# Kernel optimization log

Hardware: AMD Instinct MI355X
Metric: run time of the kernel (lower is better)

The kernel has to match this reference:

```python
import jax, jax.numpy as jnp
import numpy as np

D = 768  # in_channels == out_channels (forced by residual + shared LayerNorm)
B, S = 8, 2048


def setup_inputs() -> dict:
    key = jax.random.key(0)
    ks = jax.random.split(key, 5)
    x = jax.random.normal(ks[0], (B, S, D), dtype=jnp.float32)
    # LayerNorm params
    ln_g = jnp.ones((D,), dtype=jnp.float32)
    ln_b = jnp.zeros((D,), dtype=jnp.float32)
    # Q/K linear params (torch Linear: y = x @ W.T + b)
    scale = 1.0 / np.sqrt(D)
    Wq = jax.random.uniform(ks[1], (D, D), jnp.float32, -scale, scale)
    bq = jax.random.uniform(ks[2], (D,), jnp.float32, -scale, scale)
    Wk = jax.random.uniform(ks[3], (D, D), jnp.float32, -scale, scale)
    bk = jax.random.uniform(ks[4], (D,), jnp.float32, -scale, scale)
    return {"x": x, "ln_g": ln_g, "ln_b": ln_b, "Wq": Wq, "bq": bq, "Wk": Wk, "bk": bk}


def _layernorm(x, g, b, eps=1e-5):
    mu = jnp.mean(x, axis=-1, keepdims=True)
    var = jnp.mean(jnp.square(x - mu), axis=-1, keepdims=True)
    return (x - mu) * jax.lax.rsqrt(var + eps) * g + b


def reference(x, ln_g, ln_b, Wq, bq, Wk, bk):
    origin = x
    xn = _layernorm(x, ln_g, ln_b)
    Q = xn @ Wq.T + bq  # [B,S,D]
    K = xn @ Wk.T + bk  # [B,S,D]
    scores = jnp.einsum('bsd,btd->bst', Q, K) / jnp.sqrt(jnp.asarray(D, x.dtype))
    attn = jax.nn.softmax(scores, axis=-1)  # [B,S,S]
    out = jnp.einsum('bst,btd->bsd', attn, origin) + origin
    # note: original then computes relu(layernorm(out)) but returns `out` (dead code)
    return out
```

## Files before the change

### kernel.cpp

```cpp
#include <hip/hip_runtime.h>

typedef __bf16 bf16;
typedef __bf16 v8bf __attribute__((ext_vector_type(8)));
typedef __bf16 v4bf __attribute__((ext_vector_type(4)));
typedef float  v4f  __attribute__((ext_vector_type(4)));

__device__ __forceinline__ void gload_lds16(const void* g, void* l) {
    __builtin_amdgcn_global_load_lds(
        (const __attribute__((address_space(1))) void*)g,
        (__attribute__((address_space(3))) void*)l, 16, 0, 0);
}

#define MFMA16(a, b, c) __builtin_amdgcn_mfma_f32_16x16x32_bf16((a), (b), (c), 0, 0, 0)

__global__ __launch_bounds__(256)
void ln_cast(const float* __restrict__ x, const float* __restrict__ g,
             const float* __restrict__ b, bf16* __restrict__ xn,
             bf16* __restrict__ xv, float* __restrict__ L)
{
    const long row = blockIdx.x;
    const float* xr = x + row * 768;
    const int tid = threadIdx.x;
    const int wave = tid >> 6, lane = tid & 63;

    if (row < 64) L[row * 256 + tid] = 0.0f;

    float a0 = xr[tid], a1 = xr[tid + 256], a2 = xr[tid + 512];
    float s = a0 + a1 + a2;
    #pragma unroll
    for (int off = 32; off; off >>= 1) s += __shfl_xor(s, off);
    __shared__ float sh[4], sh2[4];
    if (!lane) sh[wave] = s;
    __syncthreads();
    const float mu = (sh[0] + sh[1] + sh[2] + sh[3]) * (1.0f / 768.0f);

    float d0 = a0 - mu, d1 = a1 - mu, d2 = a2 - mu;
    float ss = d0 * d0 + d1 * d1 + d2 * d2;
    #pragma unroll
    for (int off = 32; off; off >>= 1) ss += __shfl_xor(ss, off);
    if (!lane) sh2[wave] = ss;
    __syncthreads();
    const float var = (sh2[0] + sh2[1] + sh2[2] + sh2[3]) * (1.0f / 768.0f);
    const float rstd = rsqrtf(var + 1e-5f);

    bf16* xnr = xn + row * 768;
    bf16* xvr = xv + row * 768;
    xnr[tid]       = (bf16)(d0 * rstd * g[tid]       + b[tid]);
    xnr[tid + 256] = (bf16)(d1 * rstd * g[tid + 256] + b[tid + 256]);
    xnr[tid + 512] = (bf16)(d2 * rstd * g[tid + 512] + b[tid + 512]);
    xvr[tid]       = (bf16)a0;
    xvr[tid + 256] = (bf16)a1;
    xvr[tid + 512] = (bf16)a2;
}

__global__ __launch_bounds__(256)
void cvt_w(const float* __restrict__ Wq, const float* __restrict__ Wk,
           bf16* __restrict__ Wcat)
{
    const int z = blockIdx.y;
    const float* src = z ? Wk : Wq;
    bf16* dst = Wcat + (long)z * 768 * 768;
    const int i = (blockIdx.x * 256 + threadIdx.x) * 4;
    const float4 v = *(const float4*)(src + i);
    v4bf o = {(bf16)v.x, (bf16)v.y, (bf16)v.z, (bf16)v.w};
    *(v4bf*)(dst + i) = o;
}

__global__ __launch_bounds__(256)
void transpose_bf(const bf16* __restrict__ in, bf16* __restrict__ outT)
{
    __shared__ __attribute__((aligned(16))) bf16 tile[64 * 64];
    const int t0 = blockIdx.x * 64, d0 = blockIdx.y * 64;
    in   += (long)blockIdx.z * 2048 * 768;
    outT += (long)blockIdx.z * 768 * 2048;
    const int tid = threadIdx.x;

    #pragma unroll
    for (int it = 0; it < 2; ++it) {
        const int lin = it * 256 + tid;
        const int r = lin >> 3;
        const int g = lin & 7;
        const int pg = g ^ (r & 7) ^ ((r >> 3) & 7);
        v8bf v = *(const v8bf*)(in + (long)(t0 + r) * 768 + d0 + g * 8);
        *(v8bf*)(tile + r * 64 + pg * 8) = v;
    }
    __syncthreads();
    #pragma unroll
    for (int it = 0; it < 2; ++it) {
        const int lin = it * 256 + tid;
        const int dd = lin >> 3;
        const int tb = lin & 7;
        v8bf o;
        #pragma unroll
        for (int j = 0; j < 8; ++j) {
            const int t = tb * 8 + j;
            const int pg = (dd >> 3) ^ (t & 7) ^ ((t >> 3) & 7);
            o[j] = tile[t * 64 + pg * 8 + (dd & 7)];
        }
        *(v8bf*)(outT + (long)(d0 + dd) * 2048 + t0 + tb * 8) = o;
    }
}

__global__ __launch_bounds__(256)
void gemm_qk(const bf16* __restrict__ A, const bf16* __restrict__ W,
             const float* __restrict__ bq, const float* __restrict__ bk,
             float qscale, bf16* __restrict__ Qb, bf16* __restrict__ Kb)
{
    __shared__ __attribute__((aligned(16))) bf16 As[2][128 * 32];
    __shared__ __attribute__((aligned(16))) bf16 Bs[2][128 * 32];

    const int bx = blockIdx.x;
    const int r = bx & 7, j = bx >> 3;
    const int m0 = (r * 16 + j / 12) * 128;
    const int n0 = (j % 12) * 128;

    const int tid = threadIdx.x, wave = tid >> 6, lane = tid & 63;
    const bf16* Ab = A + (long)m0 * 768;
    const bf16* Bb = W + (long)n0 * 768;

    const int lrow = lane >> 2;
    const int lk   = (lane & 3) * 8;
    const int wm = (wave >> 1) * 64, wn = (wave & 1) * 64;
    const int lr = lane & 15, lq = lane >> 4;

    v4f acc[4][4] = {};

    for (int kk = 0; kk < 768; kk += 64) {
        #pragma unroll
        for (int p = 0; p < 2; ++p)
            #pragma unroll
            for (int it = 0; it < 2; ++it) {
                const int c = it * 4 + wave;
                const int row = c * 16 + lrow;
                gload_lds16(Ab + (long)row * 768 + kk + p * 32 + lk,
                            (char*)As[p] + c * 1024);
                gload_lds16(Bb + (long)row * 768 + kk + p * 32 + lk,
                            (char*)Bs[p] + c * 1024);
            }
        __syncthreads();

        #pragma unroll
        for (int p = 0; p < 2; ++p) {
            v8bf af[4], bfr[4];
            #pragma unroll
            for (int i = 0; i < 4; ++i)
                af[i] = *(const v8bf*)(As[p] + (wm + i * 16 + lr) * 32 + lq * 8);
            #pragma unroll
            for (int jj = 0; jj < 4; ++jj)
                bfr[jj] = *(const v8bf*)(Bs[p] + (wn + jj * 16 + lr) * 32 + lq * 8);
            #pragma unroll
            for (int i = 0; i < 4; ++i)
                #pragma unroll
                for (int jj = 0; jj < 4; ++jj)
                    acc[i][jj] = MFMA16(af[i], bfr[jj], acc[i][jj]);
        }
        __syncthreads();
    }

    const bool isQ = (n0 < 768);
    const float* bias = isQ ? bq : bk;
    const float sc = isQ ? qscale : 1.0f;
    bf16* C = isQ ? Qb : Kb;
    const int c0 = isQ ? n0 : n0 - 768;

    #pragma unroll
    for (int i = 0; i < 4; ++i) {
        #pragma unroll
        for (int rr = 0; rr < 4; ++rr) {
            const int row = m0 + wm + i * 16 + lq * 4 + rr;
            #pragma unroll
            for (int jj = 0; jj < 4; ++jj) {
                const int col = c0 + wn + jj * 16 + lr;
                C[(long)row * 768 + col] = (bf16)((acc[i][jj][rr] + bias[col]) * sc);
            }
        }
    }
}

__global__ __launch_bounds__(512, 2)
void gemm_scores(const bf16* __restrict__ Q, const bf16* __restrict__ K,
                 bf16* __restrict__ E, float* __restrict__ L)
{
    __shared__ __attribute__((aligned(16))) bf16 lds[2][32768];

    const int bx = blockIdx.x;
    const int batch = bx & 7, j = bx >> 3;
    const int m0 = (j >> 3) * 256, n0 = (j & 7) * 256;

    const bf16* Ag = Q + (long)batch * 2048 * 768 + (long)m0 * 768;
    const bf16* Bg = K + (long)batch * 2048 * 768 + (long)n0 * 768;
    bf16* C = E + (long)batch * 2048 * 2048;
    float* Lb = L + (long)batch * 2048;

    const int tid = threadIdx.x, wv = tid >> 6, lane = tid & 63;
    const int wr = wv >> 2, wc = wv & 3;
    const int lr = lane & 15, lq = lane >> 4;

    auto stA = [&](int bi, int h, int p, int kk) {
        const int lin = (wv * 2 + p) * 64 + lane;
        const int r = lin >> 3, ck = (lin & 7) ^ (r & 7);
        gload_lds16(Ag + (long)(h * 128 + r) * 768 + kk + ck * 8,
                    (char*)lds + bi * 65536 + h * 16384 + lin * 16);
    };
    auto stB = [&](int bi, int h, int p, int kk) {
        const int lin = (wv * 2 + p) * 64 + lane;
        const int r = lin >> 3, ck = (lin & 7) ^ (r & 7);
        gload_lds16(Bg + (long)(h * 128 + r) * 768 + kk + ck * 8,
                    (char*)lds + bi * 65536 + 32768 + h * 16384 + lin * 16);
    };

    v8bf a[4][2], b[2][2];
    v4f acc[2][2][4][2] = {};

    auto rdA = [&](const bf16* Ls, int mh) {
        #pragma unroll
        for (int i = 0; i < 4; ++i) {
            const int r = mh * 128 + wr * 64 + i * 16 + lr;
            #pragma unroll
            for (int s = 0; s < 2; ++s)
                a[i][s] = *(const v8bf*)(Ls + r * 64 + (((s * 4 + lq) ^ (r & 7)) << 3));
        }
    };
    auto rdB = [&](const bf16* Ls, int nh) {
        #pragma unroll
        for (int n = 0; n < 2; ++n) {
            const int r = nh * 128 + wc * 32 + n * 16 + lr;
            #pragma unroll
            for (int s = 0; s < 2; ++s)
                b[n][s] = *(const v8bf*)(Ls + 16384 + r * 64 + (((s * 4 + lq) ^ (r & 7)) << 3));
        }
    };
    auto mm = [&](v4f (&ac)[4][2]) {
        __builtin_amdgcn_s_setprio(1);
        #pragma unroll
        for (int s = 0; s < 2; ++s)
            #pragma unroll
            for (int i = 0; i < 4; ++i)
                #pragma unroll
                for (int n = 0; n < 2; ++n)
                    ac[i][n] = MFMA16(a[i][s], b[n][s], ac[i][n]);
        __builtin_amdgcn_s_setprio(0);
    };

    const int NT = 12;
    stA(0, 0, 0, 0); stA(0, 0, 1, 0); stB(0, 0, 0, 0); stB(0, 0, 1, 0);
    stA(0, 1, 0, 0); stA(0, 1, 1, 0); stB(0, 1, 0, 0); stB(0, 1, 1, 0);
    asm volatile("s_waitcnt vmcnt(4)" ::: "memory");
    __builtin_amdgcn_s_barrier();

    for (int t = 0; t < NT; ++t) {
        const int cur = t & 1, nxt = cur ^ 1;
        const int kk2 = (t + 1 < NT ? t + 1 : NT - 1) * 64;
        const bf16* Ls = lds[cur];

        rdA(Ls, 0); rdB(Ls, 0);
        stA(nxt, 0, 0, kk2); stA(nxt, 0, 1, kk2);
        __builtin_amdgcn_s_barrier();
        mm(acc[0][0]);
        asm volatile("s_waitcnt vmcnt(4)" ::: "memory");
        __builtin_amdgcn_s_barrier();

        rdA(Ls, 1);
        stB(nxt, 0, 0, kk2); stB(nxt, 0, 1, kk2);
        __builtin_amdgcn_s_barrier();
        mm(acc[1][0]);
        asm volatile("s_waitcnt vmcnt(4)" ::: "memory");
        __builtin_amdgcn_s_barrier();

        rdB(Ls, 1);
        stA(nxt, 1, 0, kk2); stA(nxt, 1, 1, kk2);
        __builtin_amdgcn_s_barrier();
        mm(acc[1][1]);
        __builtin_amdgcn_s_barrier();

        rdA(Ls, 0);
        stB(nxt, 1, 0, kk2); stB(nxt, 1, 1, kk2);
        __builtin_amdgcn_s_barrier();
        mm(acc[0][1]);
        asm volatile("s_waitcnt vmcnt(4)" ::: "memory");
        __builtin_amdgcn_s_barrier();
    }
    asm volatile("s_waitcnt vmcnt(0)" ::: "memory");

    #pragma unroll
    for (int mh = 0; mh < 2; ++mh)
    #pragma unroll
    for (int i = 0; i < 4; ++i) {
        #pragma unroll
        for (int rr = 0; rr < 4; ++rr) {
            const int row = m0 + mh * 128 + wr * 64 + i * 16 + lq * 4 + rr;
            float e[4], rs = 0.f;
            #pragma unroll
            for (int nh = 0; nh < 2; ++nh)
                #pragma unroll
                for (int n = 0; n < 2; ++n) {
                    e[nh * 2 + n] = __expf(acc[mh][nh][i][n][rr]);
                    rs += e[nh * 2 + n];
                }
            #pragma unroll
            for (int off = 1; off < 16; off <<= 1) rs += __shfl_xor(rs, off);
            if (lr == 0) atomicAdd(&Lb[row], rs);
            #pragma unroll
            for (int nh = 0; nh < 2; ++nh)
                #pragma unroll
                for (int n = 0; n < 2; ++n) {
                    const int col = n0 + nh * 128 + wc * 32 + n * 16 + lr;
                    C[(long)row * 2048 + col] = (bf16)e[nh * 2 + n];
                }
        }
    }
}

__global__ __launch_bounds__(512, 2)
void gemm_pv(const bf16* __restrict__ P, const bf16* __restrict__ VT,
             const float* __restrict__ L, const float* __restrict__ Xres,
             float* __restrict__ Out)
{
    __shared__ __attribute__((aligned(16))) bf16 lds[2][32768];

    const int bx = blockIdx.x;
    const int batch = bx & 7, j = bx >> 3;
    const int m0 = (j >> 1) * 128;
    const int n0 = (j & 1) * 384;

    const bf16* Ag = P  + (long)batch * 2048 * 2048 + (long)m0 * 2048;
    const bf16* Bg = VT + (long)batch * 768 * 2048  + (long)n0 * 2048;
    const float* Lb = L + (long)batch * 2048;
    const float* Xr = Xres + (long)batch * 2048 * 768;
    float* O = Out + (long)batch * 2048 * 768;

    const int tid = threadIdx.x, wv = tid >> 6, lane = tid & 63;
    const int wr = wv >> 2, wc = wv & 3;
    const int lr = lane & 15, lq = lane >> 4;

    auto stA = [&](int bi, int h, int kk) {
        const int lin = wv * 64 + lane;
        const int r = lin >> 3, ck = (lin & 7) ^ (r & 7);
        gload_lds16(Ag + (long)(h * 64 + r) * 2048 + kk + ck * 8,
                    (char*)lds + bi * 65536 + h * 8192 + lin * 16);
    };
    auto stB = [&](int bi, int h, int p, int kk) {
        const int lin = (wv * 3 + p) * 64 + lane;
        const int r = lin >> 3, ck = (lin & 7) ^ (r & 7);
        gload_lds16(Bg + (long)(h * 192 + r) * 2048 + kk + ck * 8,
                    (char*)lds + bi * 65536 + 16384 + h * 24576 + lin * 16);
    };

    v8bf a[2][2], b[3][2];
    v4f acc[2][2][2][3] = {};

    auto rdA = [&](const bf16* Ls, int mh) {
        #pragma unroll
        for (int i = 0; i < 2; ++i) {
            const int r = mh * 64 + wr * 32 + i * 16 + lr;
            #pragma unroll
            for (int s = 0; s < 2; ++s)
                a[i][s] = *(const v8bf*)(Ls + r * 64 + (((s * 4 + lq) ^ (r & 7)) << 3));
        }
    };
    auto rdB = [&](const bf16* Ls, int nh) {
        #pragma unroll
        for (int n = 0; n < 3; ++n) {
            const int r = nh * 192 + wc * 48 + n * 16 + lr;
            #pragma unroll
            for (int s = 0; s < 2; ++s)
                b[n][s] = *(const v8bf*)(Ls + 8192 + r * 64 + (((s * 4 + lq) ^ (r & 7)) << 3));
        }
    };
    auto mm = [&](v4f (&ac)[2][3]) {
        __builtin_amdgcn_s_setprio(1);
        #pragma unroll
        for (int s = 0; s < 2; ++s)
            #pragma unroll
            for (int i = 0; i < 2; ++i)
                #pragma unroll
                for (int n = 0; n < 3; ++n)
                    ac[i][n] = MFMA16(a[i][s], b[n][s], ac[i][n]);
        __builtin_amdgcn_s_setprio(0);
    };

    const int NT = 32;
    stA(0, 0, 0); stB(0, 0, 0, 0); stB(0, 0, 1, 0); stB(0, 0, 2, 0);
    stA(0, 1, 0); stB(0, 1, 0, 0); stB(0, 1, 1, 0); stB(0, 1, 2, 0);
    asm volatile("s_waitcnt vmcnt(4)" ::: "memory");
    __builtin_amdgcn_s_barrier();

    for (int t = 0; t < NT; ++t) {
        const int cur = t & 1, nxt = cur ^ 1;
        const int kk2 = (t + 1 < NT ? t + 1 : NT - 1) * 64;
        const bf16* Ls = lds[cur];

        rdA(Ls, 0); rdB(Ls, 0);
        stA(nxt, 0, kk2); stB(nxt, 0, 0, kk2);
        __builtin_amdgcn_s_barrier();
        mm(acc[0][0]);
        asm volatile("s_waitcnt vmcnt(5)" ::: "memory");
        __builtin_amdgcn_s_barrier();

        rdA(Ls, 1);
        stB(nxt, 0, 1, kk2); stB(nxt, 0, 2, kk2);
        __builtin_amdgcn_s_barrier();
        mm(acc[1][0]);
        asm volatile("s_waitcnt vmcnt(4)" ::: "memory");
        __builtin_amdgcn_s_barrier();

        rdB(Ls, 1);
        stA(nxt, 1, kk2); stB(nxt, 1, 0, kk2);
        __builtin_amdgcn_s_barrier();
        mm(acc[1][1]);
        __builtin_amdgcn_s_barrier();

        rdA(Ls, 0);
        stB(nxt, 1, 1, kk2); stB(nxt, 1, 2, kk2);
        __builtin_amdgcn_s_barrier();
        mm(acc[0][1]);
        asm volatile("s_waitcnt vmcnt(4)" ::: "memory");
        __builtin_amdgcn_s_barrier();
    }
    asm volatile("s_waitcnt vmcnt(0)" ::: "memory");

    #pragma unroll
    for (int mh = 0; mh < 2; ++mh)
    #pragma unroll
    for (int i = 0; i < 2; ++i) {
        #pragma unroll
        for (int rr = 0; rr < 4; ++rr) {
            const int row = m0 + mh * 64 + wr * 32 + i * 16 + lq * 4 + rr;
            const float invL = 1.0f / Lb[row];
            #pragma unroll
            for (int nh = 0; nh < 2; ++nh)
                #pragma unroll
                for (int n = 0; n < 3; ++n) {
                    const int col = n0 + nh * 192 + wc * 48 + n * 16 + lr;
                    const long idx = (long)row * 768 + col;
                    O[idx] = acc[mh][nh][i][n][rr] * invL + Xr[idx];
                }
        }
    }
}

extern "C" void kernel_launch(void* const* d_in, const int* in_sizes, int n_in,
                              void* d_out, int out_size, void* d_ws, size_t ws_size,
                              hipStream_t stream)
{
    const float* x    = (const float*)d_in[0];
    const float* ln_g = (const float*)d_in[1];
    const float* ln_b = (const float*)d_in[2];
    const float* Wq   = (const float*)d_in[3];
    const float* bq   = (const float*)d_in[4];
    const float* Wk   = (const float*)d_in[5];
    const float* bk   = (const float*)d_in[6];
    float* out = (float*)d_out;

    const long R = 8L * 2048;
    char* ws = (char*)d_ws;
    size_t off = 0;
    auto take = [&](size_t bytes) -> char* {
        char* p = ws + off;
        off += (bytes + 255) & ~(size_t)255;
        return p;
    };
    bf16*  xn   = (bf16*)take(R * 768 * 2);
    bf16*  xv   = (bf16*)take(R * 768 * 2);
    bf16*  Qb   = (bf16*)take(R * 768 * 2);
    bf16*  Kb   = (bf16*)take(R * 768 * 2);
    bf16*  Wcat = (bf16*)take(1536L * 768 * 2);
    float* Lrow = (float*)take(R * 4);
    bf16*  Sc   = (bf16*)take(8L * 2048 * 2048 * 2);

    ln_cast<<<R, 256, 0, stream>>>(x, ln_g, ln_b, xn, xv, Lrow);
    cvt_w<<<dim3(576, 2), 256, 0, stream>>>(Wq, Wk, Wcat);

    const float qscale = 0.036084391824351615f;
    gemm_qk<<<1536, 256, 0, stream>>>(xn, Wcat, bq, bk, qscale, Qb, Kb);

    bf16* xvT = xn;
    transpose_bf<<<dim3(32, 12, 8), 256, 0, stream>>>(xv, xvT);

    gemm_scores<<<512, 512, 0, stream>>>(Qb, Kb, Sc, Lrow);
    gemm_pv<<<256, 512, 0, stream>>>(Sc, xvT, Lrow, x, out);
}
```

Baseline: 312.1 us.

## Retile QK projection GEMM and software-pipeline LDS fragment reads across all GEMMs

The Q/K projection GEMM moves from a simple 128x128 double-buffered loop to a 128x384 tile with 512 threads, reusing the same swizzled 4-phase pipeline as the PV GEMM. In all three GEMMs, LDS fragment reads for the next phase are issued before the current MFMA block, including prefetching the next k-tile's first fragments, and some barriers are removed. The goal is to hide LDS read latency behind MFMAs and cut barrier stalls. The cost is more registers from the extra fragment buffers, and the vmcnt/barrier ordering needs care to stay correct.

```diff
diff --git a/kernel.cpp b/kernel.cpp
--- a/kernel.cpp
+++ b/kernel.cpp
@@ -101,61 +101,108 @@
     }
 }
 
-__global__ __launch_bounds__(256)
+__global__ __launch_bounds__(512, 2)
 void gemm_qk(const bf16* __restrict__ A, const bf16* __restrict__ W,
              const float* __restrict__ bq, const float* __restrict__ bk,
              float qscale, bf16* __restrict__ Qb, bf16* __restrict__ Kb)
 {
-    __shared__ __attribute__((aligned(16))) bf16 As[2][128 * 32];
-    __shared__ __attribute__((aligned(16))) bf16 Bs[2][128 * 32];
+    __shared__ __attribute__((aligned(16))) bf16 lds[2][32768];
 
     const int bx = blockIdx.x;
-    const int r = bx & 7, j = bx >> 3;
-    const int m0 = (r * 16 + j / 12) * 128;
-    const int n0 = (j % 12) * 128;
-
-    const int tid = threadIdx.x, wave = tid >> 6, lane = tid & 63;
-    const bf16* Ab = A + (long)m0 * 768;
-    const bf16* Bb = W + (long)n0 * 768;
-
-    const int lrow = lane >> 2;
-    const int lk   = (lane & 3) * 8;
-    const int wm = (wave >> 1) * 64, wn = (wave & 1) * 64;
+    const int wg = (bx & 7) * 64 + (bx >> 3);
+    const int m0 = (wg >> 2) * 128;
+    const int n0 = (wg & 3) * 384;
+
+    const bf16* Ag = A + (long)m0 * 768;
+    const bf16* Bg = W + (long)n0 * 768;
+
+    const int tid = threadIdx.x, wv = tid >> 6, lane = tid & 63;
+    const int wr = wv >> 2, wc = wv & 3;
     const int lr = lane & 15, lq = lane >> 4;
 
-    v4f acc[4][4] = {};
-
-    for (int kk = 0; kk < 768; kk += 64) {
-        #pragma unroll
-        for (int p = 0; p < 2; ++p)
-            #pragma unroll
-            for (int it = 0; it < 2; ++it) {
-                const int c = it * 4 + wave;
-                const int row = c * 16 + lrow;
-                gload_lds16(Ab + (long)row * 768 + kk + p * 32 + lk,
-                            (char*)As[p] + c * 1024);
-                gload_lds16(Bb + (long)row * 768 + kk + p * 32 + lk,
-                            (char*)Bs[p] + c * 1024);
-            }
-        __syncthreads();
-
-        #pragma unroll
-        for (int p = 0; p < 2; ++p) {
-            v8bf af[4], bfr[4];
-            #pragma unroll
-            for (int i = 0; i < 4; ++i)
-                af[i] = *(const v8bf*)(As[p] + (wm + i * 16 + lr) * 32 + lq * 8);
-            #pragma unroll
-            for (int jj = 0; jj < 4; ++jj)
-                bfr[jj] = *(const v8bf*)(Bs[p] + (wn + jj * 16 + lr) * 32 + lq * 8);
-            #pragma unroll
-            for (int i = 0; i < 4; ++i)
-                #pragma unroll
-                for (int jj = 0; jj < 4; ++jj)
-                    acc[i][jj] = MFMA16(af[i], bfr[jj], acc[i][jj]);
-        }
-        __syncthreads();
-    }
+    auto stA = [&](int bi, int h, int kk) {
+        const int lin = wv * 64 + lane;
+        const int r = lin >> 3, ck = (lin & 7) ^ (r & 7);
+        gload_lds16(Ag + (long)(h * 64 + r) * 768 + kk + ck * 8,
+                    (char*)lds + bi * 65536 + h * 8192 + lin * 16);
+    };
+    auto stB = [&](int bi, int h, int p, int kk) {
+        const int lin = (wv * 3 + p) * 64 + lane;
+        const int r = lin >> 3, ck = (lin & 7) ^ (r & 7);
+        gload_lds16(Bg + (long)(h * 192 + r) * 768 + kk + ck * 8,
+                    (char*)lds + bi * 65536 + 16384 + h * 24576 + lin * 16);
+    };
+
+    v8bf aS1[2][2], aS2[2][2], aS3[2][2], bS4[3][2], bS5[3][2];
+    v4f acc[2][2][2][3] = {};
+
+    auto rdA = [&](v8bf (&d)[2][2], const bf16* Ls, int mh) {
+        #pragma unroll
+        for (int i = 0; i < 2; ++i) {
+            const int r = mh * 64 + wr * 32 + i * 16 + lr;
+            #pragma unroll
+            for (int s = 0; s < 2; ++s)
+                d[i][s] = *(const v8bf*)(Ls + r * 64 + (((s * 4 + lq) ^ (r & 7)) << 3));
+        }
+    };
+    auto rdB = [&](v8bf (&d)[3][2], const bf16* Ls, int nh) {
+        #pragma unroll
+        for (int n = 0; n < 3; ++n) {
+            const int r = nh * 192 + wc * 48 + n * 16 + lr;
+            #pragma unroll
+            for (int s = 0; s < 2; ++s)
+                d[n][s] = *(const v8bf*)(Ls + 8192 + r * 64 + (((s * 4 + lq) ^ (r & 7)) << 3));
+        }
+    };
+    auto mm = [&](v8bf (&a)[2][2], v8bf (&b)[3][2], v4f (&ac)[2][3]) {
+        __builtin_amdgcn_s_setprio(1);
+        #pragma unroll
+        for (int s = 0; s < 2; ++s)
+            #pragma unroll
+            for (int i = 0; i < 2; ++i)
+                #pragma unroll
+                for (int n = 0; n < 3; ++n)
+                    ac[i][n] = MFMA16(a[i][s], b[n][s], ac[i][n]);
+        __builtin_amdgcn_s_setprio(0);
+    };
+
+    const int NT = 12;
+    stA(0, 0, 0); stB(0, 0, 0, 0); stB(0, 0, 1, 0); stB(0, 0, 2, 0);
+    stA(0, 1, 0); stB(0, 1, 0, 0); stB(0, 1, 1, 0); stB(0, 1, 2, 0);
+    asm volatile("s_waitcnt vmcnt(3)" ::: "memory");
+    __builtin_amdgcn_s_barrier();
+    rdA(aS1, lds[0], 0); rdB(bS4, lds[0], 0);
+
+    for (int t = 0; t < NT; ++t) {
+        const int cur = t & 1, nxt = cur ^ 1;
+        const int kk2 = (t + 1 < NT ? t + 1 : t) * 64;
+        const bf16* Ls = lds[cur];
+        const bf16* Ln = lds[nxt];
+
+        rdA(aS2, Ls, 1);
+        stA(nxt, 0, kk2);
+        mm(aS1, bS4, acc[0][0]);
+        asm volatile("s_waitcnt vmcnt(1)" ::: "memory");
+        __builtin_amdgcn_s_barrier();
+
+        rdB(bS5, Ls, 1);
+        stB(nxt, 0, 0, kk2); stB(nxt, 0, 1, kk2); stB(nxt, 0, 2, kk2);
+        mm(aS2, bS4, acc[1][0]);
+        __builtin_amdgcn_s_barrier();
+
+        rdA(aS3, Ls, 0);
+        stA(nxt, 1, kk2);
+        mm(aS2, bS5, acc[1][1]);
+        asm volatile("s_waitcnt vmcnt(1)" ::: "memory");
+        __builtin_amdgcn_s_barrier();
+
+        rdA(aS1, Ln, 0); rdB(bS4, Ln, 0);
+        stB(nxt, 1, 0, kk2); stB(nxt, 1, 1, kk2); stB(nxt, 1, 2, kk2);
+        mm(aS3, bS5, acc[0][1]);
+        asm volatile("s_waitcnt vmcnt(3)" ::: "memory");
+        __builtin_amdgcn_s_barrier();
+    }
+    asm volatile("s_waitcnt vmcnt(0)" ::: "memory");
 
     const bool isQ = (n0 < 768);
     const float* bias = isQ ? bq : bk;
@@ -164,15 +211,19 @@
     const int c0 = isQ ? n0 : n0 - 768;
 
     #pragma unroll
-    for (int i = 0; i < 4; ++i) {
+    for (int mh = 0; mh < 2; ++mh)
+    #pragma unroll
+    for (int i = 0; i < 2; ++i) {
         #pragma unroll
         for (int rr = 0; rr < 4; ++rr) {
-            const int row = m0 + wm + i * 16 + lq * 4 + rr;
-            #pragma unroll
-            for (int jj = 0; jj < 4; ++jj) {
-                const int col = c0 + wn + jj * 16 + lr;
-                C[(long)row * 768 + col] = (bf16)((acc[i][jj][rr] + bias[col]) * sc);
-            }
+            const int row = m0 + mh * 64 + wr * 32 + i * 16 + lq * 4 + rr;
+            #pragma unroll
+            for (int nh = 0; nh < 2; ++nh)
+                #pragma unroll
+                for (int n = 0; n < 3; ++n) {
+                    const int col = c0 + nh * 192 + wc * 48 + n * 16 + lr;
+                    C[(long)row * 768 + col] = (bf16)((acc[mh][nh][i][n][rr] + bias[col]) * sc);
+                }
         }
     }
 }
@@ -209,28 +260,28 @@
                     (char*)lds + bi * 65536 + 32768 + h * 16384 + lin * 16);
     };
 
-    v8bf a[4][2], b[2][2];
+    v8bf aS1[4][2], aS2[4][2], aS3[4][2], bS4[2][2], bS5[2][2];
     v4f acc[2][2][4][2] = {};
 
-    auto rdA = [&](const bf16* Ls, int mh) {
+    auto rdA = [&](v8bf (&d)[4][2], const bf16* Ls, int mh) {
         #pragma unroll
         for (int i = 0; i < 4; ++i) {
             const int r = mh * 128 + wr * 64 + i * 16 + lr;
             #pragma unroll
             for (int s = 0; s < 2; ++s)
-                a[i][s] = *(const v8bf*)(Ls + r * 64 + (((s * 4 + lq) ^ (r & 7)) << 3));
-        }
-    };
-    auto rdB = [&](const bf16* Ls, int nh) {
+                d[i][s] = *(const v8bf*)(Ls + r * 64 + (((s * 4 + lq) ^ (r & 7)) << 3));
+        }
+    };
+    auto rdB = [&](v8bf (&d)[2][2], const bf16* Ls, int nh) {
         #pragma unroll
         for (int n = 0; n < 2; ++n) {
             const int r = nh * 128 + wc * 32 + n * 16 + lr;
             #pragma unroll
             for (int s = 0; s < 2; ++s)
-                b[n][s] = *(const v8bf*)(Ls + 16384 + r * 64 + (((s * 4 + lq) ^ (r & 7)) << 3));
-        }
-    };
-    auto mm = [&](v4f (&ac)[4][2]) {
+                d[n][s] = *(const v8bf*)(Ls + 16384 + r * 64 + (((s * 4 + lq) ^ (r & 7)) << 3));
+        }
+    };
+    auto mm = [&](v8bf (&a)[4][2], v8bf (&b)[2][2], v4f (&ac)[4][2]) {
         __builtin_amdgcn_s_setprio(1);
         #pragma unroll
         for (int s = 0; s < 2; ++s)
@@ -245,39 +296,38 @@
     const int NT = 12;
     stA(0, 0, 0, 0); stA(0, 0, 1, 0); stB(0, 0, 0, 0); stB(0, 0, 1, 0);
     stA(0, 1, 0, 0); stA(0, 1, 1, 0); stB(0, 1, 0, 0); stB(0, 1, 1, 0);
-    asm volatile("s_waitcnt vmcnt(4)" ::: "memory");
+    asm volatile("s_waitcnt vmcnt(2)" ::: "memory");
     __builtin_amdgcn_s_barrier();
+    rdA(aS1, lds[0], 0); rdB(bS4, lds[0], 0);
 
     for (int t = 0; t < NT; ++t) {
         const int cur = t & 1, nxt = cur ^ 1;
-        const int kk2 = (t + 1 < NT ? t + 1 : NT - 1) * 64;
+        const int kk2 = (t + 1 < NT ? t + 1 : t) * 64;
         const bf16* Ls = lds[cur];
-
-        rdA(Ls, 0); rdB(Ls, 0);
+        const bf16* Ln = lds[nxt];
+
+        rdA(aS2, Ls, 1);
         stA(nxt, 0, 0, kk2); stA(nxt, 0, 1, kk2);
-        __builtin_amdgcn_s_barrier();
-        mm(acc[0][0]);
-        asm volatile("s_waitcnt vmcnt(4)" ::: "memory");
-        __builtin_amdgcn_s_barrier();
-
-        rdA(Ls, 1);
+        mm(aS1, bS4, acc[0][0]);
+        asm volatile("s_waitcnt vmcnt(2)" ::: "memory");
+        __builtin_amdgcn_s_barrier();
+
+        rdB(bS5, Ls, 1);
         stB(nxt, 0, 0, kk2); stB(nxt, 0, 1, kk2);
-        __builtin_amdgcn_s_barrier();
-        mm(acc[1][0]);
-        asm volatile("s_waitcnt vmcnt(4)" ::: "memory");
-        __builtin_amdgcn_s_barrier();
-
-        rdB(Ls, 1);
+        mm(aS2, bS4, acc[1][0]);
+        asm volatile("s_waitcnt vmcnt(2)" ::: "memory");
+        __builtin_amdgcn_s_barrier();
+
+        rdA(aS3, Ls, 0);
         stA(nxt, 1, 0, kk2); stA(nxt, 1, 1, kk2);
-        __builtin_amdgcn_s_barrier();
-        mm(acc[1][1]);
-        __builtin_amdgcn_s_barrier();
-
-        rdA(Ls, 0);
+        mm(aS2, bS5, acc[1][1]);
+        asm volatile("s_waitcnt vmcnt(2)" ::: "memory");
+        __builtin_amdgcn_s_barrier();
+
+        rdA(aS1, Ln, 0); rdB(bS4, Ln, 0);
         stB(nxt, 1, 0, kk2); stB(nxt, 1, 1, kk2);
-        __builtin_amdgcn_s_barrier();
-        mm(acc[0][1]);
-        asm volatile("s_waitcnt vmcnt(4)" ::: "memory");
+        mm(aS3, bS5, acc[0][1]);
+        asm volatile("s_waitcnt vmcnt(2)" ::: "memory");
         __builtin_amdgcn_s_barrier();
     }
     asm volatile("s_waitcnt vmcnt(0)" ::: "memory");
@@ -346,28 +396,28 @@
                     (char*)lds + bi * 65536 + 16384 + h * 24576 + lin * 16);
     };
 
-    v8bf a[2][2], b[3][2];
+    v8bf aS1[2][2], aS2[2][2], aS3[2][2], bS4[3][2], bS5[3][2];
     v4f acc[2][2][2][3] = {};
 
-    auto rdA = [&](const bf16* Ls, int mh) {
+    auto rdA = [&](v8bf (&d)[2][2], const bf16* Ls, int mh) {
         #pragma unroll
         for (int i = 0; i < 2; ++i) {
             const int r = mh * 64 + wr * 32 + i * 16 + lr;
             #pragma unroll
             for (int s = 0; s < 2; ++s)
-                a[i][s] = *(const v8bf*)(Ls + r * 64 + (((s * 4 + lq) ^ (r & 7)) << 3));
-        }
-    };
-    auto rdB = [&](const bf16* Ls, int nh) {
+                d[i][s] = *(const v8bf*)(Ls + r * 64 + (((s * 4 + lq) ^ (r & 7)) << 3));
+        }
+    };
+    auto rdB = [&](v8bf (&d)[3][2], const bf16* Ls, int nh) {
         #pragma unroll
         for (int n = 0; n < 3; ++n) {
             const int r = nh * 192 + wc * 48 + n * 16 + lr;
             #pragma unroll
             for (int s = 0; s < 2; ++s)
-                b[n][s] = *(const v8bf*)(Ls + 8192 + r * 64 + (((s * 4 + lq) ^ (r & 7)) << 3));
-        }
-    };
-    auto mm = [&](v4f (&ac)[2][3]) {
+                d[n][s] = *(const v8bf*)(Ls + 8192 + r * 64 + (((s * 4 + lq) ^ (r & 7)) << 3));
+        }
+    };
+    auto mm = [&](v8bf (&a)[2][2], v8bf (&b)[3][2], v4f (&ac)[2][3]) {
         __builtin_amdgcn_s_setprio(1);
         #pragma unroll
         for (int s = 0; s < 2; ++s)
@@ -382,39 +432,37 @@
     const int NT = 32;
     stA(0, 0, 0); stB(0, 0, 0, 0); stB(0, 0, 1, 0); stB(0, 0, 2, 0);
     stA(0, 1, 0); stB(0, 1, 0, 0); stB(0, 1, 1, 0); stB(0, 1, 2, 0);
-    asm volatile("s_waitcnt vmcnt(4)" ::: "memory");
+    asm volatile("s_waitcnt vmcnt(3)" ::: "memory");
     __builtin_amdgcn_s_barrier();
+    rdA(aS1, lds[0], 0); rdB(bS4, lds[0], 0);
 
     for (int t = 0; t < NT; ++t) {
         const int cur = t & 1, nxt = cur ^ 1;
-        const int kk2 = (t + 1 < NT ? t + 1 : NT - 1) * 64;
+        const int kk2 = (t + 1 < NT ? t + 1 : t) * 64;
         const bf16* Ls = lds[cur];
-
-        rdA(Ls, 0); rdB(Ls, 0);
-        stA(nxt, 0, kk2); stB(nxt, 0, 0, kk2);
-        __builtin_amdgcn_s_barrier();
-        mm(acc[0][0]);
-        asm volatile("s_waitcnt vmcnt(5)" ::: "memory");
-        __builtin_amdgcn_s_barrier();
-
-        rdA(Ls, 1);
-        stB(nxt, 0, 1, kk2); stB(nxt, 0, 2, kk2);
-        __builtin_amdgcn_s_barrier();
-        mm(acc[1][0]);
-        asm volatile("s_waitcnt vmcnt(4)" ::: "memory");
-        __builtin_amdgcn_s_barrier();
-
-        rdB(Ls, 1);
-        stA(nxt, 1, kk2); stB(nxt, 1, 0, kk2);
-        __builtin_amdgcn_s_barrier();
-        mm(acc[1][1]);
-        __builtin_amdgcn_s_barrier();
-
-        rdA(Ls, 0);
-        stB(nxt, 1, 1, kk2); stB(nxt, 1, 2, kk2);
-        __builtin_amdgcn_s_barrier();
-        mm(acc[0][1]);
-        asm volatile("s_waitcnt vmcnt(4)" ::: "memory");
+        const bf16* Ln = lds[nxt];
+
+        rdA(aS2, Ls, 1);
+        stA(nxt, 0, kk2);
+        mm(aS1, bS4, acc[0][0]);
+        asm volatile("s_waitcnt vmcnt(1)" ::: "memory");
+        __builtin_amdgcn_s_barrier();
+
+        rdB(bS5, Ls, 1);
+        stB(nxt, 0, 0, kk2); stB(nxt, 0, 1, kk2); stB(nxt, 0, 2, kk2);
+        mm(aS2, bS4, acc[1][0]);
+        __builtin_amdgcn_s_barrier();
+
+        rdA(aS3, Ls, 0);
+        stA(nxt, 1, kk2);
+        mm(aS2, bS5, acc[1][1]);
+        asm volatile("s_waitcnt vmcnt(1)" ::: "memory");
+        __builtin_amdgcn_s_barrier();
+
+        rdA(aS1, Ln, 0); rdB(bS4, Ln, 0);
+        stB(nxt, 1, 0, kk2); stB(nxt, 1, 1, kk2); stB(nxt, 1, 2, kk2);
+        mm(aS3, bS5, acc[0][1]);
+        asm volatile("s_waitcnt vmcnt(3)" ::: "memory");
         __builtin_amdgcn_s_barrier();
     }
     asm volatile("s_waitcnt vmcnt(0)" ::: "memory");
@@ -472,7 +520,7 @@
     cvt_w<<<dim3(576, 2), 256, 0, stream>>>(Wq, Wk, Wcat);
 
     const float qscale = 0.036084391824351615f;
-    gemm_qk<<<1536, 256, 0, stream>>>(xn, Wcat, bq, bk, qscale, Qb, Kb);
+    gemm_qk<<<512, 512, 0, stream>>>(xn, Wcat, bq, bk, qscale, Qb, Kb);
 
     bf16* xvT = xn;
     transpose_bf<<<dim3(32, 12, 8), 256, 0, stream>>>(xv, xvT);
```

Result: slower. 369.7 us (+18.5%).
